# Kernel optimization log

Measured on AMD Instinct MI355X. Metric: run time of the kernel, lower is better.

## Reference

```python
import jax, jax.numpy as jnp
import numpy as np
import math

H = 8          # num_heads
HD = 16        # head_dim = attention_dim // (2*num_heads) = 256 // 16
E_SUB = 256
E_GENE = 256
DEPTH = 1
LAMBDA_INIT = 0.8 - 0.6 * math.exp(-0.3 * DEPTH)
EPS_SM = 1e-20
EPS_RMS = 1e-5


def setup_inputs() -> dict:
    key = jax.random.key(0)
    ks = jax.random.split(key, 12)
    B, S, P, G = 4, 512, 64, 32
    d2 = 2 * H * HD  # 256
    inp = {
        'query': jax.random.normal(ks[0], (B, S, E_SUB), jnp.float32),
        'key': jax.random.normal(ks[1], (B, P, G, E_GENE), jnp.float32),
        'query_mask': jnp.ones((B, S), dtype=bool),
        'key_mask': jnp.ones((B, P, G), dtype=bool),
        'Wq': jax.random.normal(ks[2], (E_SUB, d2), jnp.float32) / np.sqrt(E_SUB),
        'Wk': jax.random.normal(ks[3], (E_GENE, d2), jnp.float32) / np.sqrt(E_GENE),
        'Wv': jax.random.normal(ks[4], (E_GENE, d2), jnp.float32) / np.sqrt(E_GENE),
        'Wo': jax.random.normal(ks[5], (d2, E_SUB), jnp.float32) / np.sqrt(d2),
        'lq1': 0.1 * jax.random.normal(ks[6], (HD,), jnp.float32),
        'lk1': 0.1 * jax.random.normal(ks[7], (HD,), jnp.float32),
        'lq2': 0.1 * jax.random.normal(ks[8], (HD,), jnp.float32),
        'lk2': 0.1 * jax.random.normal(ks[9], (HD,), jnp.float32),
        'g': jnp.ones((2 * HD,), jnp.float32),  # RMSNorm weight
    }
    return inp


def _stable_softmax(x):
    x = x.astype(jnp.float32)
    m = jnp.max(x, axis=-1, keepdims=True)
    e = jnp.exp(x - m)
    return e / (jnp.sum(e, axis=-1, keepdims=True) + EPS_SM)


def reference(query, key, query_mask, key_mask, Wq, Wk, Wv, Wo, lq1, lk1, lq2, lk2, g):
    B, S, _ = query.shape
    _, P, G, Ek = key.shape
    Lk = P * G
    scaling = HD ** -0.5
    key_flat = key.reshape(B, Lk, Ek)
    # [B, H, 2, S/Lk, HD]
    Q = (query @ Wq).reshape(B, S, H, 2, HD).transpose(0, 2, 3, 1, 4) * scaling
    K = (key_flat @ Wk).reshape(B, Lk, H, 2, HD).transpose(0, 2, 3, 1, 4)
    V = (key_flat @ Wv).reshape(B, Lk, H, 2, HD).transpose(0, 2, 3, 1, 4)
    # dual-slot scores [B, H, 2, S, Lk]
    scores = jnp.einsum('bhtsd,bhtld->bhtsl', Q, K)
    mask = query_mask[:, None, None, :, None] & key_mask.reshape(B, Lk)[:, None, None, None, :]
    scores = jnp.where(mask, scores, jnp.float32(-1e20))
    scores = _stable_softmax(scores)
    lam1 = jnp.exp(jnp.sum(lq1 * lk1))
    lam2 = jnp.exp(jnp.sum(lq2 * lk2))
    lam_full = lam1 - lam2 + LAMBDA_INIT
    diff_attn = scores[:, :, 0] - lam_full * scores[:, :, 1]  # [B,H,S,Lk]
    V_cat = V.transpose(0, 1, 3, 2, 4).reshape(B, H, Lk, 2 * HD)
    out = jnp.einsum('bhsl,bhld->bhsd', diff_attn, V_cat)
    # RMSNorm over last dim, then scale
    rms = jax.lax.rsqrt(jnp.mean(out * out, axis=-1, keepdims=True) + EPS_RMS)
    out = out * rms * g * (1.0 - LAMBDA_INIT)
    out = out.transpose(0, 2, 1, 3).reshape(B, S, 2 * H * HD) @ Wo
    return out, diff_attn.reshape(B, H, S, P, G)
```

## Files before the change

### kernel.cpp

```cpp
#include <hip/hip_runtime.h>
#include <hip/hip_bf16.h>


typedef float  f32x4  __attribute__((ext_vector_type(4)));
typedef float  f32x16 __attribute__((ext_vector_type(16)));
typedef short  s16x8  __attribute__((ext_vector_type(8)));
typedef unsigned short u16;
typedef unsigned short u16x4 __attribute__((ext_vector_type(4)));
typedef unsigned int   u32;
typedef unsigned int   u32x2 __attribute__((ext_vector_type(2)));
typedef unsigned int   u32x4 __attribute__((ext_vector_type(4)));

#define LAMBDA_INIT   0.35550906759096926f
#define ONE_MINUS_LI  0.6444909324090307f
#define QSCALE        0.36067376022224085f

__device__ __forceinline__ u16 f2b(float x) {
  unsigned u = __float_as_uint(x);
  u += 0x7FFFu + ((u >> 16) & 1u);
  return (u16)(u >> 16);
}

__device__ __forceinline__ u32 cvtpk(float lo, float hi) {
  u32 r;
  asm("v_cvt_pk_bf16_f32 %0, %1, %2" : "=v"(r) : "v"(lo), "v"(hi));
  return r;
}

__device__ __forceinline__ float fexp2(float x) {
  return __builtin_amdgcn_exp2f(x);
}

__global__ __launch_bounds__(256) void prep_kernel(
    const float* __restrict__ Wq, const float* __restrict__ Wk,
    const float* __restrict__ Wv, const float* __restrict__ Wo,
    const float* __restrict__ lq1, const float* __restrict__ lk1,
    const float* __restrict__ lq2, const float* __restrict__ lk2,
    u16* __restrict__ Wqt, u16* __restrict__ Wkt,
    u16* __restrict__ Wvt, u16* __restrict__ Wot,
    float* __restrict__ lamv) {
  int i = blockIdx.x * 256 + threadIdx.x;
  int w = i >> 16, e = i & 65535;
  int n = e >> 8, k = e & 255;
  const float* W = (w == 0) ? Wq : (w == 1) ? Wk : (w == 2) ? Wv : Wo;
  u16* Wt = (w == 0) ? Wqt : (w == 1) ? Wkt : (w == 2) ? Wvt : Wot;
  Wt[e] = f2b(W[k * 256 + n]);
  if (i == 0) {
    float a1 = 0.f, a2 = 0.f;
#pragma unroll
    for (int j = 0; j < 16; ++j) { a1 += lq1[j] * lk1[j]; a2 += lq2[j] * lk2[j]; }
    lamv[0] = expf(a1) - expf(a2) + LAMBDA_INIT;
  }
}

__global__ __launch_bounds__(256) void proj_kernel(
    const float* __restrict__ query, const float* __restrict__ key,
    const u16* __restrict__ Wqt, const u16* __restrict__ Wkt,
    const u16* __restrict__ Wvt,
    u16* __restrict__ Qs, u16* __restrict__ Ks, u16* __restrict__ Vt) {
  const int z = blockIdx.z;
  if (z == 0 && blockIdx.x >= 32) return;
  const float* A  = (z == 0) ? query : key;
  const u16*   Bt = (z == 0) ? Wqt : (z == 1) ? Wkt : Wvt;
  u16*         Out = (z == 0) ? Qs : (z == 1) ? Ks : Vt;
  const float scale = (z == 0) ? QSCALE : 1.0f;

  __shared__ u16 ldsA[64][40];
  __shared__ u16 ldsB[64][40];
  const int m0 = blockIdx.x * 64, n0 = blockIdx.y * 64;
  const int tid = threadIdx.x;
  const int w = tid >> 6, lane = tid & 63;
  const int wm = (w >> 1) * 32, wn = (w & 1) * 32;
  const int c = lane & 15, q = lane >> 4;
  const int lr = tid >> 2, lc = (tid & 3) * 8;
  f32x4 acc[2][2] = {};
  const float* aptr = A + (size_t)(m0 + lr) * 256 + lc;
  const u16*   bptr = Bt + (size_t)(n0 + lr) * 256 + lc;

  f32x4 a0 = *reinterpret_cast<const f32x4*>(aptr);
  f32x4 a1 = *reinterpret_cast<const f32x4*>(aptr + 4);
  s16x8 bF = *reinterpret_cast<const s16x8*>(bptr);
  for (int k0 = 0; k0 < 256; k0 += 32) {
    u16x4 p0 = {f2b(a0[0]), f2b(a0[1]), f2b(a0[2]), f2b(a0[3])};
    u16x4 p1 = {f2b(a1[0]), f2b(a1[1]), f2b(a1[2]), f2b(a1[3])};
    *reinterpret_cast<u16x4*>(&ldsA[lr][lc]) = p0;
    *reinterpret_cast<u16x4*>(&ldsA[lr][lc + 4]) = p1;
    *reinterpret_cast<s16x8*>(&ldsB[lr][lc]) = bF;
    __syncthreads();
    if (k0 + 32 < 256) {
      a0 = *reinterpret_cast<const f32x4*>(aptr + k0 + 32);
      a1 = *reinterpret_cast<const f32x4*>(aptr + k0 + 36);
      bF = *reinterpret_cast<const s16x8*>(bptr + k0 + 32);
    }
    s16x8 af0 = *reinterpret_cast<const s16x8*>(&ldsA[wm + c][q * 8]);
    s16x8 af1 = *reinterpret_cast<const s16x8*>(&ldsA[wm + 16 + c][q * 8]);
    s16x8 bf0 = *reinterpret_cast<const s16x8*>(&ldsB[wn + c][q * 8]);
    s16x8 bf1 = *reinterpret_cast<const s16x8*>(&ldsB[wn + 16 + c][q * 8]);
    acc[0][0] = __builtin_amdgcn_mfma_f32_16x16x32_bf16(af0, bf0, acc[0][0], 0, 0, 0);
    acc[0][1] = __builtin_amdgcn_mfma_f32_16x16x32_bf16(af0, bf1, acc[0][1], 0, 0, 0);
    acc[1][0] = __builtin_amdgcn_mfma_f32_16x16x32_bf16(af1, bf0, acc[1][0], 0, 0, 0);
    acc[1][1] = __builtin_amdgcn_mfma_f32_16x16x32_bf16(af1, bf1, acc[1][1], 0, 0, 0);
    __syncthreads();
  }
#pragma unroll
  for (int mf = 0; mf < 2; ++mf)
#pragma unroll
    for (int nf = 0; nf < 2; ++nf) {
      int m = m0 + wm + mf * 16 + q * 4;
      int n = n0 + wn + nf * 16 + c;
      int hh = n >> 5, dd = n & 31;
      if (z == 2) {
        int bb = m >> 11, l = m & 2047;
        int t = l >> 4, u = l & 15;
        u16x4 pk = {f2b(acc[mf][nf][0]), f2b(acc[mf][nf][1]),
                    f2b(acc[mf][nf][2]), f2b(acc[mf][nf][3])};
        size_t idx = (((size_t)((bb * 8 + hh) * 128 + t)) * 32 + dd) * 16 + u;
        *reinterpret_cast<u16x4*>(Out + idx) = pk;
      } else {
#pragma unroll
        for (int r = 0; r < 4; ++r) {
          int mm = m + r;
          size_t idx;
          if (z == 0) {
            int bb = mm >> 9, s = mm & 511;
            idx = ((size_t)((bb * 8 + hh) * 512 + s)) * 32 + dd;
          } else {
            int bb = mm >> 11, l = mm & 2047;
            idx = ((size_t)((bb * 8 + hh) * 2048 + l)) * 32 + dd;
          }
          Out[idx] = f2b(acc[mf][nf][r] * scale);
        }
      }
    }
}

__global__ __launch_bounds__(512, 4) void attn_fused_kernel(
    const u16* __restrict__ Qs, const u16* __restrict__ Ks,
    const u16* __restrict__ Vt, const float* __restrict__ lamv,
    const float* __restrict__ g,
    float* __restrict__ diff_out, u16* __restrict__ normed) {
  __shared__ float psum[8][2][32];
  __shared__ float avred[8][16][64];
  const int i = blockIdx.x;
  const int xcd = i & 7, j = i >> 3;
  const int bh = xcd * 4 + (j >> 4);
  const int st = j & 15;
  const int b = bh >> 3, h = bh & 7;
  const int tid = threadIdx.x, w = tid >> 6, lane = tid & 63;
  const int ln = lane & 31, hi = lane >> 5;
  const int lbase = w * 256;
  const float lam = lamv[0];

  const u16* qptr = Qs + ((size_t)((b * 8 + h) * 512 + st * 32 + ln)) * 32 + hi * 8;
  const s16x8 qf0 = *reinterpret_cast<const s16x8*>(qptr);
  const s16x8 qf1 = *reinterpret_cast<const s16x8*>(qptr + 16);
  const u16* kbase = Ks + ((size_t)((b * 8 + h) * 2048)) * 32 + hi * 8;
  const u16* vbase = Vt + ((size_t)(b * 8 + h)) * 65536 + ln * 16 + hi * 8;

  float s0 = 0.f, s1 = 0.f;
  {
    const u16* kptr = kbase + (size_t)(lbase + ln) * 32;
    s16x8 kf0 = *reinterpret_cast<const s16x8*>(kptr);
    s16x8 kf1 = *reinterpret_cast<const s16x8*>(kptr + 16);
    for (int l0 = lbase; l0 < lbase + 256; l0 += 32) {
      const int lnext = (l0 + 32 < lbase + 256) ? l0 + 32 : lbase;
      const u16* knext = kbase + (size_t)(lnext + ln) * 32;
      s16x8 nf0 = *reinterpret_cast<const s16x8*>(knext);
      s16x8 nf1 = *reinterpret_cast<const s16x8*>(knext + 16);
      f32x16 c0 = {}, c1 = {};
      c0 = __builtin_amdgcn_mfma_f32_32x32x16_bf16(kf0, qf0, c0, 0, 0, 0);
      c1 = __builtin_amdgcn_mfma_f32_32x32x16_bf16(kf1, qf1, c1, 0, 0, 0);
#pragma unroll
      for (int r = 0; r < 16; ++r) { s0 += fexp2(c0[r]); s1 += fexp2(c1[r]); }
      kf0 = nf0; kf1 = nf1;
    }
  }
  s0 += __shfl_xor(s0, 32);
  s1 += __shfl_xor(s1, 32);
  if (lane < 32) { psum[w][0][lane] = s0; psum[w][1][lane] = s1; }
  __syncthreads();
  float t0 = 0.f, t1 = 0.f;
#pragma unroll
  for (int ww = 0; ww < 8; ++ww) { t0 += psum[ww][0][ln]; t1 += psum[ww][1][ln]; }
  const float r0 = 1.f / (t0 + 1e-20f);
  const float r1 = lam / (t1 + 1e-20f);

  f32x16 avacc = {};
  float* orow = diff_out +
      ((size_t)((b * 8 + h) * 512 + st * 32 + ln)) * 2048 + 4 * hi;
  {
    const u16* kptr = kbase + (size_t)(lbase + ln) * 32;
    s16x8 kf0 = *reinterpret_cast<const s16x8*>(kptr);
    s16x8 kf1 = *reinterpret_cast<const s16x8*>(kptr + 16);
    s16x8 vf0 = *reinterpret_cast<const s16x8*>(vbase + (size_t)((lbase >> 4) + 0) * 512);
    s16x8 vf1 = *reinterpret_cast<const s16x8*>(vbase + (size_t)((lbase >> 4) + 1) * 512);
    for (int l0 = lbase; l0 < lbase + 256; l0 += 32) {
      const int lnext = (l0 + 32 < lbase + 256) ? l0 + 32 : lbase;
      const u16* knext = kbase + (size_t)(lnext + ln) * 32;
      s16x8 nk0 = *reinterpret_cast<const s16x8*>(knext);
      s16x8 nk1 = *reinterpret_cast<const s16x8*>(knext + 16);
      s16x8 nv0 = *reinterpret_cast<const s16x8*>(vbase + (size_t)((lnext >> 4) + 0) * 512);
      s16x8 nv1 = *reinterpret_cast<const s16x8*>(vbase + (size_t)((lnext >> 4) + 1) * 512);
      f32x16 c0 = {}, c1 = {};
      c0 = __builtin_amdgcn_mfma_f32_32x32x16_bf16(kf0, qf0, c0, 0, 0, 0);
      c1 = __builtin_amdgcn_mfma_f32_32x32x16_bf16(kf1, qf1, c1, 0, 0, 0);
      f32x16 d;
#pragma unroll
      for (int r = 0; r < 16; ++r)
        d[r] = fexp2(c0[r]) * r0 - fexp2(c1[r]) * r1;
#pragma unroll
      for (int gq = 0; gq < 4; ++gq) {
        f32x4 v = {d[4 * gq + 0], d[4 * gq + 1], d[4 * gq + 2], d[4 * gq + 3]};
        *reinterpret_cast<f32x4*>(orow + l0 + 8 * gq) = v;
      }
#pragma unroll
      for (int sub = 0; sub < 2; ++sub) {
        u32 W0 = cvtpk(d[8 * sub + 0], d[8 * sub + 1]);
        u32 W1 = cvtpk(d[8 * sub + 2], d[8 * sub + 3]);
        u32 W2 = cvtpk(d[8 * sub + 4], d[8 * sub + 5]);
        u32 W3 = cvtpk(d[8 * sub + 6], d[8 * sub + 7]);
        u32x2 p02 = __builtin_amdgcn_permlane32_swap(W0, W2, false, false);
        u32x2 p13 = __builtin_amdgcn_permlane32_swap(W1, W3, false, false);
        union { u32x4 u; s16x8 s; } frag;
        frag.u = (u32x4){p02[0], p13[0], p02[1], p13[1]};
        s16x8 vf = (sub == 0) ? vf0 : vf1;
        avacc = __builtin_amdgcn_mfma_f32_32x32x16_bf16(vf, frag.s, avacc, 0, 0, 0);
      }
      kf0 = nk0; kf1 = nk1; vf0 = nv0; vf1 = nv1;
    }
  }

#pragma unroll
  for (int r = 0; r < 16; ++r) avred[w][r][lane] = avacc[r];
  __syncthreads();
  if (w < 4) {
#pragma unroll
    for (int r = 0; r < 16; ++r) {
      avacc[r] += avred[w + 4][r][lane];
      avred[w][r][lane] = avacc[r];
    }
  }
  __syncthreads();
  if (w < 2) {
#pragma unroll
    for (int r = 0; r < 16; ++r) {
      avacc[r] += avred[w + 2][r][lane];
      avred[w][r][lane] = avacc[r];
    }
  }
  __syncthreads();
  if (w == 0) {
#pragma unroll
    for (int r = 0; r < 16; ++r) avacc[r] += avred[1][r][lane];
    float ss = 0.f;
#pragma unroll
    for (int r = 0; r < 16; ++r) ss += avacc[r] * avacc[r];
    ss += __shfl_xor(ss, 32);
    const float sc = rsqrtf(ss * (1.f / 32.f) + 1e-5f) * ONE_MINUS_LI;
    u16* nrow = normed + ((size_t)(b * 512 + st * 32 + ln)) * 256 + h * 32 + 4 * hi;
#pragma unroll
    for (int rg = 0; rg < 4; ++rg) {
      const float* gp = g + 8 * rg + 4 * hi;
      u16x4 pk = {f2b(avacc[4 * rg + 0] * sc * gp[0]),
                  f2b(avacc[4 * rg + 1] * sc * gp[1]),
                  f2b(avacc[4 * rg + 2] * sc * gp[2]),
                  f2b(avacc[4 * rg + 3] * sc * gp[3])};
      *reinterpret_cast<u16x4*>(nrow + 8 * rg) = pk;
    }
  }
}

__global__ __launch_bounds__(256) void gemmo_kernel(
    const u16* __restrict__ A, const u16* __restrict__ Bt,
    float* __restrict__ Out) {
  __shared__ u16 ldsA[64][40];
  __shared__ u16 ldsB[64][40];
  const int m0 = blockIdx.x * 64, n0 = blockIdx.y * 64;
  const int tid = threadIdx.x;
  const int w = tid >> 6, lane = tid & 63;
  const int wm = (w >> 1) * 32, wn = (w & 1) * 32;
  const int c = lane & 15, q = lane >> 4;
  const int lr = tid >> 2, lc = (tid & 3) * 8;
  f32x4 acc[2][2] = {};
  const u16* aptr = A + (size_t)(m0 + lr) * 256 + lc;
  const u16* bptr = Bt + (size_t)(n0 + lr) * 256 + lc;
  s16x8 aF = *reinterpret_cast<const s16x8*>(aptr);
  s16x8 bF = *reinterpret_cast<const s16x8*>(bptr);
  for (int k0 = 0; k0 < 256; k0 += 32) {
    *reinterpret_cast<s16x8*>(&ldsA[lr][lc]) = aF;
    *reinterpret_cast<s16x8*>(&ldsB[lr][lc]) = bF;
    __syncthreads();
    if (k0 + 32 < 256) {
      aF = *reinterpret_cast<const s16x8*>(aptr + k0 + 32);
      bF = *reinterpret_cast<const s16x8*>(bptr + k0 + 32);
    }
    s16x8 af0 = *reinterpret_cast<const s16x8*>(&ldsA[wm + c][q * 8]);
    s16x8 af1 = *reinterpret_cast<const s16x8*>(&ldsA[wm + 16 + c][q * 8]);
    s16x8 bf0 = *reinterpret_cast<const s16x8*>(&ldsB[wn + c][q * 8]);
    s16x8 bf1 = *reinterpret_cast<const s16x8*>(&ldsB[wn + 16 + c][q * 8]);
    acc[0][0] = __builtin_amdgcn_mfma_f32_16x16x32_bf16(af0, bf0, acc[0][0], 0, 0, 0);
    acc[0][1] = __builtin_amdgcn_mfma_f32_16x16x32_bf16(af0, bf1, acc[0][1], 0, 0, 0);
    acc[1][0] = __builtin_amdgcn_mfma_f32_16x16x32_bf16(af1, bf0, acc[1][0], 0, 0, 0);
    acc[1][1] = __builtin_amdgcn_mfma_f32_16x16x32_bf16(af1, bf1, acc[1][1], 0, 0, 0);
    __syncthreads();
  }
#pragma unroll
  for (int mf = 0; mf < 2; ++mf)
#pragma unroll
    for (int nf = 0; nf < 2; ++nf)
#pragma unroll
      for (int r = 0; r < 4; ++r) {
        int m = m0 + wm + mf * 16 + q * 4 + r;
        int n = n0 + wn + nf * 16 + c;
        Out[(size_t)m * 256 + n] = acc[mf][nf][r];
      }
}

extern "C" void kernel_launch(void* const* d_in, const int* in_sizes, int n_in,
                              void* d_out, int out_size, void* d_ws, size_t ws_size,
                              hipStream_t stream) {
  const float* query = (const float*)d_in[0];
  const float* key   = (const float*)d_in[1];
  const float* Wq  = (const float*)d_in[4];
  const float* Wk  = (const float*)d_in[5];
  const float* Wv  = (const float*)d_in[6];
  const float* Wo  = (const float*)d_in[7];
  const float* lq1 = (const float*)d_in[8];
  const float* lk1 = (const float*)d_in[9];
  const float* lq2 = (const float*)d_in[10];
  const float* lk2 = (const float*)d_in[11];
  const float* g   = (const float*)d_in[12];

  float* out  = (float*)d_out;
  float* diff = out + 524288;

  char* ws = (char*)d_ws;
  u16*   Wqt  = (u16*)(ws);
  u16*   Wkt  = (u16*)(ws + (1 << 17));
  u16*   Wvt  = (u16*)(ws + 2 * (1 << 17));
  u16*   Wot  = (u16*)(ws + 3 * (1 << 17));
  float* lamv = (float*)(ws + 4 * (1 << 17));
  u16*   Qs   = (u16*)(ws + (size_t)(1 << 20));
  u16*   Ks   = (u16*)(ws + (size_t)2 * (1 << 20));
  u16*   Vt   = (u16*)(ws + (size_t)6 * (1 << 20));
  u16*   nrm  = (u16*)(ws + (size_t)10 * (1 << 20));

  prep_kernel<<<1024, 256, 0, stream>>>(Wq, Wk, Wv, Wo, lq1, lk1, lq2, lk2,
                                        Wqt, Wkt, Wvt, Wot, lamv);
  proj_kernel<<<dim3(128, 4, 3), 256, 0, stream>>>(query, key, Wqt, Wkt, Wvt,
                                                   Qs, Ks, Vt);
  attn_fused_kernel<<<512, 512, 0, stream>>>(
      Qs, Ks, Vt, lamv, g, diff, nrm);
  gemmo_kernel<<<dim3(32, 4), 256, 0, stream>>>(nrm, Wot, out);
}
```

Before: 55.89 us.

## Transpose score MFMA so diff_out stores coalesce; rebuild P fragment via LDS

Swaps the QK^T MFMA operands so each lane holds scores for one key column across several query rows. Consecutive lanes then write contiguous addresses of the large diff_out output. The per-row normalisers are broadcast through shared memory to match the new layout. The bf16 probability fragment for the AV MFMA is now built by staging through a per-wave LDS buffer instead of permlane swaps. This adds LDS traffic and scalar conversions per tile.

```diff
diff --git a/kernel.cpp b/kernel.cpp
--- a/kernel.cpp
+++ b/kernel.cpp
@@ -8,8 +8,6 @@
 typedef unsigned short u16;
 typedef unsigned short u16x4 __attribute__((ext_vector_type(4)));
 typedef unsigned int   u32;
-typedef unsigned int   u32x2 __attribute__((ext_vector_type(2)));
-typedef unsigned int   u32x4 __attribute__((ext_vector_type(4)));
 
 #define LAMBDA_INIT   0.35550906759096926f
 #define ONE_MINUS_LI  0.6444909324090307f
@@ -19,12 +17,6 @@
   unsigned u = __float_as_uint(x);
   u += 0x7FFFu + ((u >> 16) & 1u);
   return (u16)(u >> 16);
-}
-
-__device__ __forceinline__ u32 cvtpk(float lo, float hi) {
-  u32 r;
-  asm("v_cvt_pk_bf16_f32 %0, %1, %2" : "=v"(r) : "v"(lo), "v"(hi));
-  return r;
 }
 
 __device__ __forceinline__ float fexp2(float x) {
@@ -140,7 +132,9 @@
     const float* __restrict__ g,
     float* __restrict__ diff_out, u16* __restrict__ normed) {
   __shared__ float psum[8][2][32];
+  __shared__ float rden[2][32];
   __shared__ float avred[8][16][64];
+  __shared__ u16   pbuf[8][32][40];
   const int i = blockIdx.x;
   const int xcd = i & 7, j = i >> 3;
   const int bh = xcd * 4 + (j >> 4);
@@ -184,10 +178,18 @@
   for (int ww = 0; ww < 8; ++ww) { t0 += psum[ww][0][ln]; t1 += psum[ww][1][ln]; }
   const float r0 = 1.f / (t0 + 1e-20f);
   const float r1 = lam / (t1 + 1e-20f);
+  if (w == 0 && lane < 32) { rden[0][lane] = r0; rden[1][lane] = r1; }
+  __syncthreads();
+  f32x4 rq[4], rl[4];
+#pragma unroll
+  for (int gq = 0; gq < 4; ++gq) {
+    rq[gq] = *reinterpret_cast<const f32x4*>(&rden[0][gq * 8 + 4 * hi]);
+    rl[gq] = *reinterpret_cast<const f32x4*>(&rden[1][gq * 8 + 4 * hi]);
+  }
 
   f32x16 avacc = {};
-  float* orow = diff_out +
-      ((size_t)((b * 8 + h) * 512 + st * 32 + ln)) * 2048 + 4 * hi;
+  float* obase = diff_out +
+      ((size_t)((b * 8 + h) * 512 + st * 32 + 4 * hi)) * 2048 + ln;
   {
     const u16* kptr = kbase + (size_t)(lbase + ln) * 32;
     s16x8 kf0 = *reinterpret_cast<const s16x8*>(kptr);
@@ -202,30 +204,22 @@
       s16x8 nv0 = *reinterpret_cast<const s16x8*>(vbase + (size_t)((lnext >> 4) + 0) * 512);
       s16x8 nv1 = *reinterpret_cast<const s16x8*>(vbase + (size_t)((lnext >> 4) + 1) * 512);
       f32x16 c0 = {}, c1 = {};
-      c0 = __builtin_amdgcn_mfma_f32_32x32x16_bf16(kf0, qf0, c0, 0, 0, 0);
-      c1 = __builtin_amdgcn_mfma_f32_32x32x16_bf16(kf1, qf1, c1, 0, 0, 0);
+      c0 = __builtin_amdgcn_mfma_f32_32x32x16_bf16(qf0, kf0, c0, 0, 0, 0);
+      c1 = __builtin_amdgcn_mfma_f32_32x32x16_bf16(qf1, kf1, c1, 0, 0, 0);
       f32x16 d;
 #pragma unroll
       for (int r = 0; r < 16; ++r)
-        d[r] = fexp2(c0[r]) * r0 - fexp2(c1[r]) * r1;
-#pragma unroll
-      for (int gq = 0; gq < 4; ++gq) {
-        f32x4 v = {d[4 * gq + 0], d[4 * gq + 1], d[4 * gq + 2], d[4 * gq + 3]};
-        *reinterpret_cast<f32x4*>(orow + l0 + 8 * gq) = v;
-      }
-#pragma unroll
-      for (int sub = 0; sub < 2; ++sub) {
-        u32 W0 = cvtpk(d[8 * sub + 0], d[8 * sub + 1]);
-        u32 W1 = cvtpk(d[8 * sub + 2], d[8 * sub + 3]);
-        u32 W2 = cvtpk(d[8 * sub + 4], d[8 * sub + 5]);
-        u32 W3 = cvtpk(d[8 * sub + 6], d[8 * sub + 7]);
-        u32x2 p02 = __builtin_amdgcn_permlane32_swap(W0, W2, false, false);
-        u32x2 p13 = __builtin_amdgcn_permlane32_swap(W1, W3, false, false);
-        union { u32x4 u; s16x8 s; } frag;
-        frag.u = (u32x4){p02[0], p13[0], p02[1], p13[1]};
-        s16x8 vf = (sub == 0) ? vf0 : vf1;
-        avacc = __builtin_amdgcn_mfma_f32_32x32x16_bf16(vf, frag.s, avacc, 0, 0, 0);
-      }
+        d[r] = fexp2(c0[r]) * rq[r >> 2][r & 3] - fexp2(c1[r]) * rl[r >> 2][r & 3];
+#pragma unroll
+      for (int r = 0; r < 16; ++r)
+        obase[(size_t)((r & 3) + 8 * (r >> 2)) * 2048 + l0] = d[r];
+#pragma unroll
+      for (int r = 0; r < 16; ++r)
+        pbuf[w][(r & 3) + 8 * (r >> 2) + 4 * hi][ln] = f2b(d[r]);
+      s16x8 pa0 = *reinterpret_cast<const s16x8*>(&pbuf[w][ln][hi * 8]);
+      s16x8 pa1 = *reinterpret_cast<const s16x8*>(&pbuf[w][ln][16 + hi * 8]);
+      avacc = __builtin_amdgcn_mfma_f32_32x32x16_bf16(vf0, pa0, avacc, 0, 0, 0);
+      avacc = __builtin_amdgcn_mfma_f32_32x32x16_bf16(vf1, pa1, avacc, 0, 0, 0);
       kf0 = nk0; kf1 = nk1; vf0 = nv0; vf1 = nv1;
     }
   }
```

New measurement: 54.09 us. 1.03x faster.
